# Performance work log

Measured on AMD Instinct MI355X. Metric: run time of the kernel, lower is better.

Reference implementation:

```python
import jax, jax.numpy as jnp
import numpy as np

HEADS = 8
DH = 64          # channel_head
HID = HEADS * DH # 512
QC = 256         # query_channel


def rmsnorm(x, g):
    # lucidrains-style RMSNorm over channel dim of [b, c, h, w]:
    # F.normalize(x, dim=1) * g * sqrt(C)
    n = jnp.sqrt(jnp.sum(x * x, axis=1, keepdims=True))
    x = x / jnp.maximum(n, 1e-12)
    return x * (x.shape[1] ** 0.5) * g[None, :, None, None]


def setup_inputs() -> dict:
    key = jax.random.key(0)
    ks = jax.random.split(key, 6)
    B, H, W = 8, 64, 64
    x = jax.random.normal(ks[0], (B, QC, H, W), dtype=jnp.float32)
    Wq = jax.random.normal(ks[1], (HID, QC), dtype=jnp.float32) * 0.02
    Wk = jax.random.normal(ks[2], (HID, QC), dtype=jnp.float32) * 0.02
    Wv = jax.random.normal(ks[3], (HID, QC), dtype=jnp.float32) * 0.02
    conv_w = jax.random.normal(ks[4], (QC, HID), dtype=jnp.float32) * 0.02  # 1x1 conv
    conv_b = jnp.zeros((QC,), dtype=jnp.float32)
    g_ffn = jnp.ones((QC,), dtype=jnp.float32)
    g_norm = jnp.ones((QC,), dtype=jnp.float32)
    return {"x": x, "Wq": Wq, "Wk": Wk, "Wv": Wv, "conv_w": conv_w,
            "conv_b": conv_b, "g_ffn": g_ffn, "g_norm": g_norm}


def reference(x, Wq, Wk, Wv, conv_w, conv_b, g_ffn, g_norm):
    b, c, h, w = x.shape
    n = h * w
    xn = rmsnorm(x, g_norm)                    # pre-norm; residual uses xn (x_in)
    t = xn.reshape(b, c, n).transpose(0, 2, 1)  # [b, n, c]
    q = t @ Wq.T                                # [b, n, HID]
    k = t @ Wk.T
    v = t @ Wv.T
    split = lambda z: z.reshape(b, n, HEADS, DH).transpose(0, 2, 1, 3)  # [b,h,n,d]
    q, k, v = split(q), split(k), split(v)
    q = jax.nn.softmax(q, axis=-1) * (DH ** -0.5)  # softmax over d, then scale
    k = jax.nn.softmax(k, axis=-2)                 # softmax over n
    attn = jnp.einsum('bhnd,bhne->bhde', k, v)     # K^T V, [b,h,d,d]
    out = jnp.einsum('bhnd,bhde->bhne', q, attn)   # [b,h,n,d]
    out = out.transpose(0, 2, 1, 3).reshape(b, n, HID)
    out = out.transpose(0, 2, 1).reshape(b, HID, h, w)
    out = jnp.einsum('bchw,oc->bohw', out, conv_w) + conv_b[None, :, None, None]
    out = rmsnorm(out, g_ffn)
    return out + xn
```

## Files before the change

kernel.cpp:

```cpp
#include <hip/hip_runtime.h>
#include <hip/hip_bf16.h>

#define B_ 8
#define C_ 256
#define N_ 4096
#define HID_ 512

typedef __bf16 bf16;
typedef bf16 bf16x8 __attribute__((ext_vector_type(8)));
typedef bf16 bf16x4 __attribute__((ext_vector_type(4)));
typedef float f32x4 __attribute__((ext_vector_type(4)));

#define T_OFF    0u
#define U_OFF    16777216u
#define S_OFF    17825792u
#define M2T_OFF  17973248u
#define WQ_OFF   20070400u
#define WK_OFF   20332544u
#define WV_OFF   20594688u

__device__ __forceinline__ f32x4 mfma16(bf16x8 a, bf16x8 b, f32x4 c) {
    return __builtin_amdgcn_mfma_f32_16x16x32_bf16(a, b, c, 0, 0, 0);
}

__device__ __forceinline__ void gload_lds16(const void* g, void* l) {
    __builtin_amdgcn_global_load_lds(
        (const __attribute__((address_space(1))) unsigned int*)g,
        (__attribute__((address_space(3))) unsigned int*)l, 16, 0, 0);
}

__global__ void __launch_bounds__(256, 4) k_nc(const float* __restrict__ x,
                                               const float* __restrict__ gnorm,
                                               bf16* __restrict__ t,
                                               const float* __restrict__ wq,
                                               const float* __restrict__ wk,
                                               const float* __restrict__ wv,
                                               bf16* __restrict__ oq,
                                               bf16* __restrict__ ok,
                                               bf16* __restrict__ ov,
                                               float* __restrict__ uz) {
    if (blockIdx.x >= 704) {
        const f32x4 z = {0.f, 0.f, 0.f, 0.f};
        int idx = (blockIdx.x - 704) * 256 + threadIdx.x;
        f32x4* dst = (f32x4*)uz;
#pragma unroll
        for (int i = 0; i < 9; ++i) {
            int j = idx + i * 8192;
            if (j < 66560) dst[j] = z;
        }
        return;
    }
    if (blockIdx.x >= 512) {
        int bb = blockIdx.x - 512;
        int m = bb >> 6;
        const float* src = (m == 0) ? wq : ((m == 1) ? wk : wv);
        bf16* dst = (m == 0) ? oq : ((m == 1) ? ok : ov);
        int tid = threadIdx.x;
        int i0 = ((bb & 63) * 256 + tid) * 8;
        f32x4 a = *(const f32x4*)(src + i0);
        f32x4 b2 = *(const f32x4*)(src + i0 + 4);
        bf16x8 o;
#pragma unroll
        for (int j = 0; j < 4; ++j) { o[j] = (bf16)a[j]; o[j + 4] = (bf16)b2[j]; }
        int row = (bb & 63) * 8 + (tid >> 5);
        int k0 = (tid & 31) * 8;
        int p = row >> 4, l15 = row & 15;
        int ks = k0 >> 5, g = (k0 >> 3) & 3;
        *(bf16x8*)(dst + ((size_t)((p * 8 + ks) * 64 + g * 16 + l15)) * 8) = o;
        return;
    }
    __shared__ float part[4][64];
    int b = blockIdx.x >> 6;
    int pix = ((blockIdx.x & 63) << 6) + (threadIdx.x & 63);
    int cq = threadIdx.x >> 6;
    const float* xb = x + (size_t)b * C_ * N_ + (size_t)(cq * 64) * N_ + pix;
    float xv[64];
    float ss = 0.f;
#pragma unroll
    for (int c = 0; c < 64; ++c) { xv[c] = xb[(size_t)c * N_]; ss += xv[c] * xv[c]; }
    part[cq][threadIdx.x & 63] = ss;
    __syncthreads();
    int p = threadIdx.x & 63;
    float tot = part[0][p] + part[1][p] + part[2][p] + part[3][p];
    float s = 16.0f / fmaxf(sqrtf(tot), 1e-12f);
    bf16* tb = t + ((size_t)(b * N_ + pix)) * C_ + cq * 64;
#pragma unroll
    for (int c0 = 0; c0 < 64; c0 += 8) {
        bf16x8 pk;
#pragma unroll
        for (int j = 0; j < 8; ++j)
            pk[j] = (bf16)(xv[c0 + j] * s * gnorm[cq * 64 + c0 + j]);
        *(bf16x8*)(tb + c0) = pk;
    }
}

__global__ void __launch_bounds__(256, 2) k_kv(const bf16* __restrict__ t,
                                               const bf16* __restrict__ wkb,
                                               const bf16* __restrict__ wvb,
                                               float* __restrict__ U,
                                               float* __restrict__ S) {
    __shared__ __align__(16) bf16 tS[64 * 256];
    __shared__ __align__(16) bf16 ekT[64][72];
    __shared__ __align__(16) bf16 vT[64][72];
    int h = blockIdx.x >> 6;
    int b = (blockIdx.x >> 3) & 7;
    int chunk = blockIdx.x & 7;
    int w = threadIdx.x >> 6;
    int l = threadIdx.x & 63;
    int l15 = l & 15, g = l >> 4;
    int xorm = (l15 & 7) << 4;

    const bf16* wsel = (w < 2) ? wkb : wvb;
    int c0 = (w & 1) * 32;
    bool isk = (w < 2);
    bf16x8 wf[2][8];
#pragma unroll
    for (int nf = 0; nf < 2; ++nf) {
        int pp = h * 4 + (w & 1) * 2 + nf;
#pragma unroll
        for (int ks = 0; ks < 8; ++ks)
            wf[nf][ks] = *(const bf16x8*)(wsel + ((size_t)((pp * 8 + ks) * 64 + l)) * 8);
    }

    const f32x4 fz = {0.f, 0.f, 0.f, 0.f};
    f32x4 uacc[4];
#pragma unroll
    for (int df = 0; df < 4; ++df) uacc[df] = fz;
    float sreg = 0.f;

    size_t rowbase = (size_t)b * N_ + chunk * 512;
    for (int tile = 0; tile < 8; ++tile) {
        {
            const char* gt = (const char*)(t + (rowbase + tile * 64) * 256);
#pragma unroll
            for (int it = 0; it < 8; ++it) {
                int o = it * 4096 + w * 1024 + l * 16;
                int src = o ^ (((o >> 9) & 7) << 4);
                gload_lds16(gt + src, (char*)tS + it * 4096 + w * 1024);
            }
        }
        __syncthreads();
        f32x4 acc[4][2];
#pragma unroll
        for (int mf = 0; mf < 4; ++mf) { acc[mf][0] = fz; acc[mf][1] = fz; }
#pragma unroll
        for (int ks = 0; ks < 8; ++ks) {
#pragma unroll
            for (int mf = 0; mf < 4; ++mf) {
                bf16x8 a = *(const bf16x8*)((const char*)tS + (mf * 16 + l15) * 512 + ((ks * 64 + g * 16) ^ xorm));
                acc[mf][0] = mfma16(a, wf[0][ks], acc[mf][0]);
                acc[mf][1] = mfma16(a, wf[1][ks], acc[mf][1]);
            }
        }
        __syncthreads();
#pragma unroll
        for (int mf = 0; mf < 4; ++mf)
#pragma unroll
            for (int nf = 0; nf < 2; ++nf) {
                int cc = c0 + nf * 16 + l15;
                int rr = mf * 16 + g * 4;
                bf16x4 pk;
#pragma unroll
                for (int r = 0; r < 4; ++r) {
                    float v = acc[mf][nf][r];
                    pk[r] = (bf16)(isk ? __expf(v) : v);
                }
                if (isk) *(bf16x4*)(&ekT[cc][rr]) = pk;
                else     *(bf16x4*)(&vT[cc][rr]) = pk;
            }
        __syncthreads();
#pragma unroll
        for (int k2 = 0; k2 < 2; ++k2) {
            bf16x8 bv = *(const bf16x8*)(&vT[w * 16 + l15][k2 * 32 + g * 8]);
#pragma unroll
            for (int df = 0; df < 4; ++df) {
                bf16x8 ae = *(const bf16x8*)(&ekT[df * 16 + l15][k2 * 32 + g * 8]);
                uacc[df] = mfma16(ae, bv, uacc[df]);
            }
        }
        {
#pragma unroll
            for (int i = 0; i < 16; ++i) sreg += (float)ekT[l][w * 16 + i];
        }
    }
    int bh = b * 8 + h;
    float* Ubh = U + (size_t)bh * 4096;
#pragma unroll
    for (int df = 0; df < 4; ++df)
#pragma unroll
        for (int r = 0; r < 4; ++r)
            atomicAdd(Ubh + (df * 16 + g * 4 + r) * 64 + w * 16 + l15, uacc[df][r]);
    atomicAdd(S + bh * 64 + l, sreg);
}

__global__ void __launch_bounds__(256) k_attn_m2(const float* __restrict__ U,
                                                 const float* __restrict__ S,
                                                 const float* __restrict__ cw,
                                                 bf16* __restrict__ m2t) {
    __shared__ float at[16][64];
    int b = blockIdx.x & 7, dq = (blockIdx.x >> 3) & 3, h = blockIdx.x >> 5;
    int tid = threadIdx.x;
    const float* Ub = U + (size_t)(b * 8 + h) * 4096 + dq * 16 * 64;
    const float* Sb = S + (b * 8 + h) * 64 + dq * 16;
    for (int it = 0; it < 4; ++it) {
        int idx = it * 256 + tid;
        at[idx >> 6][idx & 63] = Ub[idx] / Sb[idx >> 6];
    }
    __syncthreads();
    int o = tid;
    float cwr[64];
#pragma unroll
    for (int e = 0; e < 64; ++e) cwr[e] = cw[(size_t)o * 512 + h * 64 + e];
    bf16* mb = m2t + (size_t)b * 131072;
    int pp = o >> 4, l15o = o & 15;
#pragma unroll
    for (int j0 = 0; j0 < 16; j0 += 8) {
        bf16x8 pk;
#pragma unroll
        for (int j = 0; j < 8; ++j) {
            float a2 = 0.f;
#pragma unroll
            for (int e = 0; e < 64; ++e) a2 += at[j0 + j][e] * cwr[e];
            pk[j] = (bf16)a2;
        }
        int kk = dq * 16 + j0;
        int ksg = h * 2 + (kk >> 5);
        int gg = (kk >> 3) & 3;
        *(bf16x8*)(mb + ((size_t)((pp * 16 + ksg) * 64 + gg * 16 + l15o)) * 8) = pk;
    }
}

__global__ void __launch_bounds__(512, 4) k_qout(const bf16* __restrict__ t,
                                                 const bf16* __restrict__ wqb,
                                                 const bf16* __restrict__ m2t,
                                                 const float* __restrict__ gffn,
                                                 const float* __restrict__ cb,
                                                 float* __restrict__ out) {
    __shared__ __align__(16) char smem[66560 + 2048];
    bf16 (*qsm)[520] = (bf16(*)[520])smem;
    float* rowsum = (float*)(smem + 66560);
    bf16* tS = (bf16*)smem;
    int b = blockIdx.x & 7;
    int row0 = (blockIdx.x >> 3) << 6;
    int tid = threadIdx.x;
    int w = tid >> 6, l = tid & 63;
    int l15 = l & 15, g = l >> 4;
    int xorm = (l15 & 7) << 4;
    const f32x4 fz = {0.f, 0.f, 0.f, 0.f};

    {
        const char* gt = (const char*)(t + (size_t)(b * N_ + row0) * 256);
#pragma unroll
        for (int it = 0; it < 4; ++it) {
            int o = it * 8192 + tid * 16;
            int src = o ^ (((o >> 9) & 7) << 4);
            gload_lds16(gt + src, (char*)tS + o);
        }
    }
    __syncthreads();

    f32x4 acc[4][4];
#pragma unroll
    for (int mf = 0; mf < 4; ++mf)
#pragma unroll
        for (int nf = 0; nf < 4; ++nf) acc[mf][nf] = fz;
#pragma unroll
    for (int ks = 0; ks < 8; ++ks) {
        bf16x8 a[4];
#pragma unroll
        for (int mf = 0; mf < 4; ++mf)
            a[mf] = *(const bf16x8*)((const char*)tS + (mf * 16 + l15) * 512 + ((ks * 64 + g * 16) ^ xorm));
#pragma unroll
        for (int nf = 0; nf < 4; ++nf) {
            bf16x8 bq = *(const bf16x8*)(wqb + ((size_t)(((w * 4 + nf) * 8 + ks) * 64 + l)) * 8);
#pragma unroll
            for (int mf = 0; mf < 4; ++mf)
                acc[mf][nf] = mfma16(a[mf], bq, acc[mf][nf]);
        }
    }
    __syncthreads();

#pragma unroll
    for (int mf = 0; mf < 4; ++mf)
#pragma unroll
        for (int r = 0; r < 4; ++r) {
            float mx = -1e30f;
#pragma unroll
            for (int nf = 0; nf < 4; ++nf) mx = fmaxf(mx, acc[mf][nf][r]);
            mx = fmaxf(mx, __shfl_xor(mx, 1));
            mx = fmaxf(mx, __shfl_xor(mx, 2));
            mx = fmaxf(mx, __shfl_xor(mx, 4));
            mx = fmaxf(mx, __shfl_xor(mx, 8));
            float p[4]; float sm = 0.f;
#pragma unroll
            for (int nf = 0; nf < 4; ++nf) { p[nf] = __expf(acc[mf][nf][r] - mx); sm += p[nf]; }
            sm += __shfl_xor(sm, 1);
            sm += __shfl_xor(sm, 2);
            sm += __shfl_xor(sm, 4);
            sm += __shfl_xor(sm, 8);
            float scl = 0.125f / sm;
            int row = mf * 16 + g * 4 + r;
#pragma unroll
            for (int nf = 0; nf < 4; ++nf)
                qsm[row][w * 64 + nf * 16 + l15] = (bf16)(p[nf] * scl);
        }
    __syncthreads();

    f32x4 acc2[4][2];
#pragma unroll
    for (int mf = 0; mf < 4; ++mf)
#pragma unroll
        for (int nf = 0; nf < 2; ++nf) acc2[mf][nf] = fz;
    const bf16* mb = m2t + (size_t)b * 131072;
#pragma unroll
    for (int ks = 0; ks < 16; ++ks) {
        bf16x8 a[4];
#pragma unroll
        for (int mf = 0; mf < 4; ++mf)
            a[mf] = *(const bf16x8*)(&qsm[mf * 16 + l15][ks * 32 + g * 8]);
#pragma unroll
        for (int nf = 0; nf < 2; ++nf) {
            bf16x8 bm = *(const bf16x8*)(mb + ((size_t)(((w * 2 + nf) * 16 + ks) * 64 + l)) * 8);
#pragma unroll
            for (int mf = 0; mf < 4; ++mf)
                acc2[mf][nf] = mfma16(a[mf], bm, acc2[mf][nf]);
        }
    }

#pragma unroll
    for (int nf = 0; nf < 2; ++nf) {
        float bias = cb[w * 32 + nf * 16 + l15];
#pragma unroll
        for (int mf = 0; mf < 4; ++mf)
#pragma unroll
            for (int r = 0; r < 4; ++r) acc2[mf][nf][r] += bias;
    }
#pragma unroll
    for (int mf = 0; mf < 4; ++mf)
#pragma unroll
        for (int r = 0; r < 4; ++r) {
            float ssq = 0.f;
#pragma unroll
            for (int nf = 0; nf < 2; ++nf) ssq += acc2[mf][nf][r] * acc2[mf][nf][r];
            ssq += __shfl_xor(ssq, 1);
            ssq += __shfl_xor(ssq, 2);
            ssq += __shfl_xor(ssq, 4);
            ssq += __shfl_xor(ssq, 8);
            if (l15 == 0) rowsum[w * 64 + mf * 16 + g * 4 + r] = ssq;
        }
    __syncthreads();
    float sclr[4][4];
#pragma unroll
    for (int mf = 0; mf < 4; ++mf)
#pragma unroll
        for (int r = 0; r < 4; ++r) {
            int row = mf * 16 + g * 4 + r;
            float tot = 0.f;
#pragma unroll
            for (int ww = 0; ww < 8; ++ww) tot += rowsum[ww * 64 + row];
            sclr[mf][r] = 16.0f / fmaxf(sqrtf(tot), 1e-12f);
        }

    float* obuf = (float*)smem;
    const bf16* gtb = t + (size_t)(b * N_ + row0) * 256;
#pragma unroll
    for (int nf = 0; nf < 2; ++nf) {
        int col = w * 32 + nf * 16 + l15;
        float gf = gffn[col];
#pragma unroll
        for (int mf = 0; mf < 4; ++mf)
#pragma unroll
            for (int r = 0; r < 4; ++r) {
                int row = mf * 16 + g * 4 + r;
                float res = (float)gtb[row * 256 + col];
                obuf[col * 65 + row] = acc2[mf][nf][r] * sclr[mf][r] * gf + res;
            }
    }
    __syncthreads();
#pragma unroll
    for (int cc = 0; cc < 8; ++cc) {
        int c = cc * 32 + (tid >> 4);
        int j = (tid & 15) * 4;
        f32x4 v;
#pragma unroll
        for (int r = 0; r < 4; ++r) v[r] = obuf[c * 65 + j + r];
        __builtin_nontemporal_store(v, (f32x4*)(out + ((size_t)(b * 256 + c)) * N_ + row0 + j));
    }
}

extern "C" void kernel_launch(void* const* d_in, const int* in_sizes, int n_in,
                              void* d_out, int out_size, void* d_ws, size_t ws_size,
                              hipStream_t stream) {
    const float* x     = (const float*)d_in[0];
    const float* Wq    = (const float*)d_in[1];
    const float* Wk    = (const float*)d_in[2];
    const float* Wv    = (const float*)d_in[3];
    const float* cw    = (const float*)d_in[4];
    const float* cb    = (const float*)d_in[5];
    const float* gffn  = (const float*)d_in[6];
    const float* gnorm = (const float*)d_in[7];
    char* ws = (char*)d_ws;
    bf16* t    = (bf16*)(ws + T_OFF);
    float* U   = (float*)(ws + U_OFF);
    float* S   = (float*)(ws + S_OFF);
    bf16* m2t  = (bf16*)(ws + M2T_OFF);
    bf16* wqb  = (bf16*)(ws + WQ_OFF);
    bf16* wkb  = (bf16*)(ws + WK_OFF);
    bf16* wvb  = (bf16*)(ws + WV_OFF);
    float* out = (float*)d_out;

    k_nc<<<736, 256, 0, stream>>>(x, gnorm, t, Wq, Wk, Wv, wqb, wkb, wvb, U);
    k_kv<<<512, 256, 0, stream>>>(t, wkb, wvb, U, S);
    k_attn_m2<<<256, 256, 0, stream>>>(U, S, cw, m2t);
    k_qout<<<512, 512, 0, stream>>>(t, wqb, m2t, gffn, cb, out);
}
```

Baseline: 91.82 us.

## Share staged token tile across two heads and prefetch next tile in k_kv

The k_kv kernel now runs 512-thread blocks that process two heads at once. Both heads share a single LDS copy of the token tile, which halves global reads of t. The load of the next tile is issued right after the projection results are written to LDS, so it overlaps the K^T V MFMA work. In exchange there are fewer, larger blocks (256 instead of 512) with a higher launch_bounds occupancy target, which may add register pressure. LDS use for the ekT/vT buffers also doubles.

```diff
diff --git a/kernel.cpp b/kernel.cpp
--- a/kernel.cpp
+++ b/kernel.cpp
@@ -94,29 +94,31 @@
     }
 }
 
-__global__ void __launch_bounds__(256, 2) k_kv(const bf16* __restrict__ t,
+__global__ void __launch_bounds__(512, 4) k_kv(const bf16* __restrict__ t,
                                                const bf16* __restrict__ wkb,
                                                const bf16* __restrict__ wvb,
                                                float* __restrict__ U,
                                                float* __restrict__ S) {
     __shared__ __align__(16) bf16 tS[64 * 256];
-    __shared__ __align__(16) bf16 ekT[64][72];
-    __shared__ __align__(16) bf16 vT[64][72];
-    int h = blockIdx.x >> 6;
+    __shared__ __align__(16) bf16 ekT[2][64][72];
+    __shared__ __align__(16) bf16 vT[2][64][72];
+    int hp = blockIdx.x >> 6;
     int b = (blockIdx.x >> 3) & 7;
     int chunk = blockIdx.x & 7;
-    int w = threadIdx.x >> 6;
-    int l = threadIdx.x & 63;
+    int tid = threadIdx.x;
+    int w = tid >> 6, l = tid & 63;
+    int wl = w & 3, hl = w >> 2;
+    int h = hp * 2 + hl;
     int l15 = l & 15, g = l >> 4;
     int xorm = (l15 & 7) << 4;
 
-    const bf16* wsel = (w < 2) ? wkb : wvb;
-    int c0 = (w & 1) * 32;
-    bool isk = (w < 2);
+    const bf16* wsel = (wl < 2) ? wkb : wvb;
+    int c0 = (wl & 1) * 32;
+    bool isk = (wl < 2);
     bf16x8 wf[2][8];
 #pragma unroll
     for (int nf = 0; nf < 2; ++nf) {
-        int pp = h * 4 + (w & 1) * 2 + nf;
+        int pp = h * 4 + (wl & 1) * 2 + nf;
 #pragma unroll
         for (int ks = 0; ks < 8; ++ks)
             wf[nf][ks] = *(const bf16x8*)(wsel + ((size_t)((pp * 8 + ks) * 64 + l)) * 8);
@@ -129,16 +131,17 @@
     float sreg = 0.f;
 
     size_t rowbase = (size_t)b * N_ + chunk * 512;
+#define STAGE(ti) { \
+    const char* gt_ = (const char*)(t + (rowbase + (ti) * 64) * 256); \
+    _Pragma("unroll") \
+    for (int it = 0; it < 4; ++it) { \
+        int o_ = it * 8192 + tid * 16; \
+        int src_ = o_ ^ (((o_ >> 9) & 7) << 4); \
+        gload_lds16(gt_ + src_, (char*)tS + o_); \
+    } }
+
+    STAGE(0);
     for (int tile = 0; tile < 8; ++tile) {
-        {
-            const char* gt = (const char*)(t + (rowbase + tile * 64) * 256);
-#pragma unroll
-            for (int it = 0; it < 8; ++it) {
-                int o = it * 4096 + w * 1024 + l * 16;
-                int src = o ^ (((o >> 9) & 7) << 4);
-                gload_lds16(gt + src, (char*)tS + it * 4096 + w * 1024);
-            }
-        }
         __syncthreads();
         f32x4 acc[4][2];
 #pragma unroll
@@ -165,31 +168,33 @@
                     float v = acc[mf][nf][r];
                     pk[r] = (bf16)(isk ? __expf(v) : v);
                 }
-                if (isk) *(bf16x4*)(&ekT[cc][rr]) = pk;
-                else     *(bf16x4*)(&vT[cc][rr]) = pk;
+                if (isk) *(bf16x4*)(&ekT[hl][cc][rr]) = pk;
+                else     *(bf16x4*)(&vT[hl][cc][rr]) = pk;
             }
         __syncthreads();
+        if (tile < 7) STAGE(tile + 1);
 #pragma unroll
         for (int k2 = 0; k2 < 2; ++k2) {
-            bf16x8 bv = *(const bf16x8*)(&vT[w * 16 + l15][k2 * 32 + g * 8]);
+            bf16x8 bv = *(const bf16x8*)(&vT[hl][wl * 16 + l15][k2 * 32 + g * 8]);
 #pragma unroll
             for (int df = 0; df < 4; ++df) {
-                bf16x8 ae = *(const bf16x8*)(&ekT[df * 16 + l15][k2 * 32 + g * 8]);
+                bf16x8 ae = *(const bf16x8*)(&ekT[hl][df * 16 + l15][k2 * 32 + g * 8]);
                 uacc[df] = mfma16(ae, bv, uacc[df]);
             }
         }
         {
 #pragma unroll
-            for (int i = 0; i < 16; ++i) sreg += (float)ekT[l][w * 16 + i];
-        }
-    }
+            for (int i = 0; i < 16; ++i) sreg += (float)ekT[hl][l][wl * 16 + i];
+        }
+    }
+#undef STAGE
     int bh = b * 8 + h;
     float* Ubh = U + (size_t)bh * 4096;
 #pragma unroll
     for (int df = 0; df < 4; ++df)
 #pragma unroll
         for (int r = 0; r < 4; ++r)
-            atomicAdd(Ubh + (df * 16 + g * 4 + r) * 64 + w * 16 + l15, uacc[df][r]);
+            atomicAdd(Ubh + (df * 16 + g * 4 + r) * 64 + wl * 16 + l15, uacc[df][r]);
     atomicAdd(S + bh * 64 + l, sreg);
 }
 
@@ -410,7 +415,7 @@
     float* out = (float*)d_out;
 
     k_nc<<<736, 256, 0, stream>>>(x, gnorm, t, Wq, Wk, Wv, wqb, wkb, wvb, U);
-    k_kv<<<512, 256, 0, stream>>>(t, wkb, wvb, U, S);
+    k_kv<<<256, 512, 0, stream>>>(t, wkb, wvb, U, S);
     k_attn_m2<<<256, 256, 0, stream>>>(U, S, cw, m2t);
     k_qout<<<512, 512, 0, stream>>>(t, wqb, m2t, gffn, cb, out);
 }
```

Measured after the change: 107.4 us. 17.0% more time.
